# Kernel tuning notes

Measured on AMD Instinct MI355X. Metric: run time of the kernel, lower is better.

The kernel has to match this reference:

```python
import jax, jax.numpy as jnp
import numpy as np

V, D, B, L = 100000, 64, 4096, 200

def setup_inputs() -> dict:
    key = jax.random.key(0)
    ks = jax.random.split(key, 10)
    s = 0.05  # keep activations in a sane range for sigmoid
    return {
        "item_ids": jax.random.randint(ks[0], (B,), 0, V),
        "history": jax.random.randint(ks[1], (B, L), 0, V),
        "hist_len": jax.random.randint(ks[2], (B,), 1, L + 1),
        "emb_table": jax.random.normal(ks[3], (V, D), jnp.float32) * s,
        "aW1": jax.random.normal(ks[4], (3 * D, D), jnp.float32) * s,
        "ab1": jnp.zeros((D,), jnp.float32),
        "aW2": jax.random.normal(ks[5], (D, 1), jnp.float32) * s,
        "ab2": jnp.zeros((1,), jnp.float32),
        "fW1": jax.random.normal(ks[6], (3 * D, 128), jnp.float32) * s,
        "fb1": jnp.zeros((128,), jnp.float32),
        "fW2": jax.random.normal(ks[7], (128, 64), jnp.float32) * s,
        "fb2": jnp.zeros((64,), jnp.float32),
        "fW3": jax.random.normal(ks[8], (64, 1), jnp.float32) * s,
        "fb3": jnp.zeros((1,), jnp.float32),
    }

def reference(item_ids, history, hist_len, emb_table, aW1, ab1, aW2, ab2,
              fW1, fb1, fW2, fb2, fW3, fb3):
    target = emb_table[item_ids]                      # [B, D]
    hist = emb_table[history]                         # [B, L, D]
    # original pads short histories with zero rows -> zero the padded tail
    mask = (jnp.arange(hist.shape[1])[None, :] < hist_len[:, None]).astype(hist.dtype)
    hist = hist * mask[..., None]
    tgt = jnp.broadcast_to(target[:, None, :], hist.shape)     # [B, L, D]
    # attention_fc takes 3*D features: (hist, target, hist*target)
    feat = jnp.concatenate([hist, tgt, hist * tgt], axis=-1)   # [B, L, 3D]
    h = jax.nn.relu(feat @ aW1 + ab1)                 # [B, L, D]
    scores = (h @ aW2 + ab2)[..., 0]                  # [B, L]
    # faithful to original: softmax over full padded length (no length mask)
    w = jax.nn.softmax(scores, axis=1)
    pooled = jnp.einsum('bl,bld->bd', w, hist)        # [B, D]
    comb = jnp.concatenate([target, pooled, pooled - target], axis=-1)  # [B, 3D]
    z = jax.nn.relu(comb @ fW1 + fb1)
    z = jax.nn.relu(z @ fW2 + fb2)
    return jax.nn.sigmoid(z @ fW3 + fb3)              # [B, 1]
```

## Files before the change

### kernel.cpp

```cpp
#include <hip/hip_runtime.h>
#include <hip/hip_bf16.h>

#define NV 100000
#define ND 64
#define NB 4096
#define NL 200
#define HST 72

typedef __bf16 bf16_t;
typedef __bf16 bf16x8 __attribute__((ext_vector_type(8)));
typedef float  f32x4  __attribute__((ext_vector_type(4)));

__global__ __launch_bounds__(256, 5)
void din_kernel1(const int* __restrict__ item_ids,
                 const int* __restrict__ history,
                 const int* __restrict__ hist_len,
                 const float* __restrict__ emb,
                 const float* __restrict__ aW1,
                 const float* __restrict__ ab1,
                 const float* __restrict__ aW2,
                 float* __restrict__ comb_ws)
{
    __shared__ __align__(16) bf16_t histA[208 * HST];
    __shared__ __align__(16) float sc_w[208];
    __shared__ float pp[256];
    __shared__ float tgt[64];
    __shared__ float cb[64];
    __shared__ float pooled[64];
    __shared__ float red[8];

    const int b    = blockIdx.x;
    const int tid  = threadIdx.x;
    const int item = item_ids[b];
    const int len  = hist_len[b];
    const int wave = tid >> 6, lane = tid & 63;
    const int col  = lane & 15, quad = lane >> 4;

    if (tid < 64) tgt[tid] = emb[(long)item * ND + tid];

    {
        const int p     = tid & 3;
        const int lbase = tid >> 2;
        int  idxs[4];
        bool vs[4];
        #pragma unroll
        for (int pass = 0; pass < 4; ++pass) {
            int l  = pass * 64 + lbase;
            int lc = l < NL ? l : NL - 1;
            idxs[pass] = history[b * NL + lc];
            vs[pass]   = l < len;
        }
        #pragma unroll
        for (int g = 0; g < 2; ++g) {
            f32x4 r[2][4];
            #pragma unroll
            for (int q = 0; q < 2; ++q) {
                int pass = g * 2 + q;
                int l = pass * 64 + lbase;
                if (l < 208 && vs[pass]) {
                    const float* src = emb + (long)idxs[pass] * ND + p * 16;
                    r[q][0] = *(const f32x4*)(src);
                    r[q][1] = *(const f32x4*)(src + 4);
                    r[q][2] = *(const f32x4*)(src + 8);
                    r[q][3] = *(const f32x4*)(src + 12);
                }
            }
            #pragma unroll
            for (int q = 0; q < 2; ++q) {
                int pass = g * 2 + q;
                int l = pass * 64 + lbase;
                if (l < 208) {
                    bf16x8 o0 = (bf16x8)(bf16_t)0.f, o1 = (bf16x8)(bf16_t)0.f;
                    if (vs[pass]) {
                        #pragma unroll
                        for (int i = 0; i < 4; ++i) {
                            o0[i]     = (bf16_t)r[q][0][i];
                            o0[i + 4] = (bf16_t)r[q][1][i];
                            o1[i]     = (bf16_t)r[q][2][i];
                            o1[i + 4] = (bf16_t)r[q][3][i];
                        }
                    }
                    bf16_t* dst = &histA[l * HST + p * 16];
                    *(bf16x8*)(dst)     = o0;
                    *(bf16x8*)(dst + 8) = o1;
                }
            }
        }
    }

    {
        const int n4 = (tid & 15) * 4;
        const int kp = tid >> 4;
        f32x4 t4  = *(const f32x4*)(emb + (long)item * ND + kp * 4);
        f32x4 wb0 = *(const f32x4*)(aW1 + (64 + kp * 4 + 0) * 64 + n4);
        f32x4 wb1 = *(const f32x4*)(aW1 + (64 + kp * 4 + 1) * 64 + n4);
        f32x4 wb2 = *(const f32x4*)(aW1 + (64 + kp * 4 + 2) * 64 + n4);
        f32x4 wb3 = *(const f32x4*)(aW1 + (64 + kp * 4 + 3) * 64 + n4);
        f32x4 c4;
        #pragma unroll
        for (int j = 0; j < 4; ++j)
            c4[j] = t4[0] * wb0[j] + t4[1] * wb1[j] + t4[2] * wb2[j] + t4[3] * wb3[j];
        #pragma unroll
        for (int j = 0; j < 4; ++j) {
            c4[j] += __shfl_xor(c4[j], 16, 64);
            c4[j] += __shfl_xor(c4[j], 32, 64);
        }
        if (lane < 16) *(f32x4*)&pp[wave * 64 + n4] = c4;
    }

    __syncthreads();

    if (tid < 64) cb[tid] = ab1[tid] + pp[tid] + pp[64 + tid] + pp[128 + tid] + pp[192 + tid];

    bf16x8 bfrag[4][2];
    #pragma unroll
    for (int kb = 0; kb < 2; ++kb) {
        f32x4 t0 = *(const f32x4*)&tgt[kb * 32 + quad * 8];
        f32x4 t1 = *(const f32x4*)&tgt[kb * 32 + quad * 8 + 4];
        #pragma unroll
        for (int nt = 0; nt < 4; ++nt) {
            const int n = nt * 16 + col;
            const float* pa = aW1 + (long)(kb * 32 + quad * 8) * 64 + n;
            const float* pc = pa + 128 * 64;
            float wa[8], wc[8];
            #pragma unroll
            for (int j = 0; j < 8; ++j) { wa[j] = pa[j * 64]; wc[j] = pc[j * 64]; }
            bf16x8 w;
            #pragma unroll
            for (int j = 0; j < 8; ++j) {
                float tk = (j < 4) ? t0[j] : t1[j - 4];
                w[j] = (bf16_t)(wa[j] + tk * wc[j]);
            }
            bfrag[nt][kb] = w;
        }
    }
    float a2vals[4];
    #pragma unroll
    for (int nt = 0; nt < 4; ++nt) a2vals[nt] = aW2[nt * 16 + col];

    __syncthreads();
    float cvals[4];
    #pragma unroll
    for (int nt = 0; nt < 4; ++nt) cvals[nt] = cb[nt * 16 + col];

    for (int mt = wave; mt < 13; mt += 4) {
        const bf16_t* arow = &histA[(mt * 16 + col) * HST + quad * 8];
        bf16x8 af0 = *(const bf16x8*)(arow);
        bf16x8 af1 = *(const bf16x8*)(arow + 32);
        float sc[4] = {0.f, 0.f, 0.f, 0.f};
        #pragma unroll
        for (int nt = 0; nt < 4; ++nt) {
            f32x4 acc = {0.f, 0.f, 0.f, 0.f};
            acc = __builtin_amdgcn_mfma_f32_16x16x32_bf16(af0, bfrag[nt][0], acc, 0, 0, 0);
            acc = __builtin_amdgcn_mfma_f32_16x16x32_bf16(af1, bfrag[nt][1], acc, 0, 0, 0);
            #pragma unroll
            for (int i = 0; i < 4; ++i) {
                float h = acc[i] + cvals[nt];
                h = h > 0.f ? h : 0.f;
                sc[i] += h * a2vals[nt];
            }
        }
        #pragma unroll
        for (int off = 1; off < 16; off <<= 1)
            #pragma unroll
            for (int i = 0; i < 4; ++i) sc[i] += __shfl_xor(sc[i], off, 64);
        if (col == 0) {
            f32x4 outv = {sc[0], sc[1], sc[2], sc[3]};
            *(f32x4*)&sc_w[mt * 16 + quad * 4] = outv;
        }
    }
    __syncthreads();

    {
        float s = (tid < NL) ? sc_w[tid] : -1e30f;
        float m = s;
        #pragma unroll
        for (int off = 32; off > 0; off >>= 1) m = fmaxf(m, __shfl_xor(m, off, 64));
        if (lane == 0) red[wave] = m;
        __syncthreads();
        m = fmaxf(fmaxf(red[0], red[1]), fmaxf(red[2], red[3]));
        float e = (tid < NL) ? __expf(s - m) : 0.f;
        float ssum = e;
        #pragma unroll
        for (int off = 32; off > 0; off >>= 1) ssum += __shfl_xor(ssum, off, 64);
        if (lane == 0) red[4 + wave] = ssum;
        __syncthreads();
        float tot = red[4] + red[5] + red[6] + red[7];
        if (tid < NL) sc_w[tid] = e / tot;
    }
    __syncthreads();

    {
        float acc = 0.f;
        for (int l = wave; l < NL; l += 4)
            acc += sc_w[l] * (float)histA[l * HST + lane];
        pp[wave * 64 + lane] = acc;
    }
    __syncthreads();
    if (tid < 64) pooled[tid] = pp[tid] + pp[64 + tid] + pp[128 + tid] + pp[192 + tid];
    __syncthreads();

    if (tid < 192) {
        float v;
        if (tid < 64)       v = tgt[tid];
        else if (tid < 128) v = pooled[tid - 64];
        else                v = pooled[tid - 128] - tgt[tid - 128];
        comb_ws[(long)b * 192 + tid] = v;
    }
}

__global__ __launch_bounds__(256)
void din_kernel2(const float* __restrict__ comb,
                 const float* __restrict__ fW1, const float* __restrict__ fb1,
                 const float* __restrict__ fW2, const float* __restrict__ fb2,
                 const float* __restrict__ fW3, const float* __restrict__ fb3,
                 float* __restrict__ out)
{
    __shared__ float combs[4 * 192];
    __shared__ float z1s[4 * 128];
    const int tid = threadIdx.x;
    const int rb  = blockIdx.x * 4;

    for (int i = tid; i < 4 * 192; i += 256) combs[i] = comb[(long)rb * 192 + i];
    __syncthreads();

    {
        const int j  = tid & 127;
        const int r0 = (tid >> 7) * 2, r1 = r0 + 1;
        float a0 = fb1[j], a1 = a0;
        #pragma unroll 4
        for (int i = 0; i < 192; ++i) {
            float w = fW1[i * 128 + j];
            a0 += combs[r0 * 192 + i] * w;
            a1 += combs[r1 * 192 + i] * w;
        }
        z1s[r0 * 128 + j] = fmaxf(a0, 0.f);
        z1s[r1 * 128 + j] = fmaxf(a1, 0.f);
    }
    __syncthreads();

    {
        const int j2 = tid & 63;
        const int r2 = tid >> 6;
        float acc = fb2[j2];
        #pragma unroll 4
        for (int i = 0; i < 128; ++i)
            acc += z1s[r2 * 128 + i] * fW2[i * 64 + j2];
        float s = fmaxf(acc, 0.f) * fW3[j2];
        #pragma unroll
        for (int off = 1; off < 64; off <<= 1) s += __shfl_xor(s, off, 64);
        if (j2 == 0) out[rb + r2] = 1.f / (1.f + __expf(-(s + fb3[0])));
    }
}

extern "C" void kernel_launch(void* const* d_in, const int* in_sizes, int n_in,
                              void* d_out, int out_size, void* d_ws, size_t ws_size,
                              hipStream_t stream) {
    const int*   item_ids = (const int*)d_in[0];
    const int*   history  = (const int*)d_in[1];
    const int*   hist_len = (const int*)d_in[2];
    const float* emb      = (const float*)d_in[3];
    const float* aW1      = (const float*)d_in[4];
    const float* ab1      = (const float*)d_in[5];
    const float* aW2      = (const float*)d_in[6];
    const float* fW1      = (const float*)d_in[8];
    const float* fb1      = (const float*)d_in[9];
    const float* fW2      = (const float*)d_in[10];
    const float* fb2      = (const float*)d_in[11];
    const float* fW3      = (const float*)d_in[12];
    const float* fb3      = (const float*)d_in[13];

    float* comb = (float*)d_ws;

    din_kernel1<<<NB, 256, 0, stream>>>(item_ids, history, hist_len, emb,
                                        aW1, ab1, aW2, comb);
    din_kernel2<<<NB / 4, 256, 0, stream>>>(comb, fW1, fb1, fW2, fb2, fW3, fb3,
                                            (float*)d_out);
}
```

Measured before the change: 166.2 us.

## Pre-convert embedding table to bf16 and gather half-width rows

Adds a pre-pass kernel that converts the whole fp32 embedding table into a bf16 copy in workspace on every call. The attention kernel then gathers history rows from that copy, halving the bytes moved per gathered row and dropping the in-kernel conversion. The price is a full read of the table plus a half-size write each call, and an extra kernel launch. The old fp32 gather path is kept as a fallback when the workspace is too small.

Result: slower. 169.6 us (+2.0%).

```diff
diff --git a/kernel.cpp b/kernel.cpp
--- a/kernel.cpp
+++ b/kernel.cpp
@@ -11,11 +11,25 @@
 typedef __bf16 bf16x8 __attribute__((ext_vector_type(8)));
 typedef float  f32x4  __attribute__((ext_vector_type(4)));
 
+__global__ __launch_bounds__(256)
+void din_cvt(const float* __restrict__ emb, bf16_t* __restrict__ embh)
+{
+    const long base = ((long)blockIdx.x * 256 + threadIdx.x) * 8;
+    f32x4 a0 = *(const f32x4*)(emb + base);
+    f32x4 a1 = *(const f32x4*)(emb + base + 4);
+    bf16x8 o;
+    #pragma unroll
+    for (int i = 0; i < 4; ++i) { o[i] = (bf16_t)a0[i]; o[i + 4] = (bf16_t)a1[i]; }
+    *(bf16x8*)(embh + base) = o;
+}
+
+template <bool BT>
 __global__ __launch_bounds__(256, 5)
 void din_kernel1(const int* __restrict__ item_ids,
                  const int* __restrict__ history,
                  const int* __restrict__ hist_len,
                  const float* __restrict__ emb,
+                 const bf16_t* __restrict__ embh,
                  const float* __restrict__ aW1,
                  const float* __restrict__ ab1,
                  const float* __restrict__ aW2,
@@ -38,16 +52,41 @@
 
     if (tid < 64) tgt[tid] = emb[(long)item * ND + tid];
 
-    {
+    if constexpr (BT) {
+        const int p  = tid & 1;
+        const int lb = tid >> 1;
+        const int l1 = 128 + lb;
+        const int i0 = history[b * NL + (lb < NL ? lb : NL - 1)];
+        const int i1 = history[b * NL + (l1 < NL ? l1 : NL - 1)];
+        const bool v0 = lb < len, v1 = l1 < len;
+        const bf16x8 z = (bf16x8)(bf16_t)0.f;
+        bf16x8 r0[4] = {z, z, z, z}, r1[4] = {z, z, z, z};
+        if (v0) {
+            const bf16_t* s = embh + (long)i0 * ND + p * 32;
+            #pragma unroll
+            for (int j = 0; j < 4; ++j) r0[j] = *(const bf16x8*)(s + j * 8);
+        }
+        if (v1) {
+            const bf16_t* s = embh + (long)i1 * ND + p * 32;
+            #pragma unroll
+            for (int j = 0; j < 4; ++j) r1[j] = *(const bf16x8*)(s + j * 8);
+        }
+        bf16_t* d0 = &histA[lb * HST + p * 32];
+        #pragma unroll
+        for (int j = 0; j < 4; ++j) *(bf16x8*)(d0 + j * 8) = r0[j];
+        if (l1 < 208) {
+            bf16_t* d1 = &histA[l1 * HST + p * 32];
+            #pragma unroll
+            for (int j = 0; j < 4; ++j) *(bf16x8*)(d1 + j * 8) = r1[j];
+        }
+    } else {
         const int p     = tid & 3;
         const int lbase = tid >> 2;
-        int  idxs[4];
-        bool vs[4];
+        int  idxs[4]; bool vs[4];
         #pragma unroll
         for (int pass = 0; pass < 4; ++pass) {
             int l  = pass * 64 + lbase;
-            int lc = l < NL ? l : NL - 1;
-            idxs[pass] = history[b * NL + lc];
+            idxs[pass] = history[b * NL + (l < NL ? l : NL - 1)];
             vs[pass]   = l < len;
         }
         #pragma unroll
@@ -55,33 +94,27 @@
             f32x4 r[2][4];
             #pragma unroll
             for (int q = 0; q < 2; ++q) {
-                int pass = g * 2 + q;
-                int l = pass * 64 + lbase;
+                int pass = g * 2 + q, l = pass * 64 + lbase;
                 if (l < 208 && vs[pass]) {
                     const float* src = emb + (long)idxs[pass] * ND + p * 16;
-                    r[q][0] = *(const f32x4*)(src);
-                    r[q][1] = *(const f32x4*)(src + 4);
-                    r[q][2] = *(const f32x4*)(src + 8);
-                    r[q][3] = *(const f32x4*)(src + 12);
+                    #pragma unroll
+                    for (int j = 0; j < 4; ++j) r[q][j] = *(const f32x4*)(src + j * 4);
                 }
             }
             #pragma unroll
             for (int q = 0; q < 2; ++q) {
-                int pass = g * 2 + q;
-                int l = pass * 64 + lbase;
+                int pass = g * 2 + q, l = pass * 64 + lbase;
                 if (l < 208) {
                     bf16x8 o0 = (bf16x8)(bf16_t)0.f, o1 = (bf16x8)(bf16_t)0.f;
                     if (vs[pass]) {
                         #pragma unroll
                         for (int i = 0; i < 4; ++i) {
-                            o0[i]     = (bf16_t)r[q][0][i];
-                            o0[i + 4] = (bf16_t)r[q][1][i];
-                            o1[i]     = (bf16_t)r[q][2][i];
-                            o1[i + 4] = (bf16_t)r[q][3][i];
+                            o0[i] = (bf16_t)r[q][0][i]; o0[i + 4] = (bf16_t)r[q][1][i];
+                            o1[i] = (bf16_t)r[q][2][i]; o1[i + 4] = (bf16_t)r[q][3][i];
                         }
                     }
                     bf16_t* dst = &histA[l * HST + p * 16];
-                    *(bf16x8*)(dst)     = o0;
+                    *(bf16x8*)(dst) = o0;
                     *(bf16x8*)(dst + 8) = o1;
                 }
             }
@@ -270,10 +303,23 @@
     const float* fW3      = (const float*)d_in[12];
     const float* fb3      = (const float*)d_in[13];
 
-    float* comb = (float*)d_ws;
-
-    din_kernel1<<<NB, 256, 0, stream>>>(item_ids, history, hist_len, emb,
-                                        aW1, ab1, aW2, comb);
-    din_kernel2<<<NB / 4, 256, 0, stream>>>(comb, fW1, fb1, fW2, fb2, fW3, fb3,
-                                            (float*)d_out);
+    const size_t embh_bytes = (size_t)NV * ND * sizeof(bf16_t);
+    const size_t comb_bytes = (size_t)NB * 192 * sizeof(float);
+    const bool   use_bt     = ws_size >= embh_bytes + comb_bytes;
+
+    if (use_bt) {
+        bf16_t* embh = (bf16_t*)d_ws;
+        float*  comb = (float*)((char*)d_ws + embh_bytes);
+        din_cvt<<<(NV * ND) / (256 * 8), 256, 0, stream>>>(emb, embh);
+        din_kernel1<true><<<NB, 256, 0, stream>>>(item_ids, history, hist_len, emb,
+                                                  embh, aW1, ab1, aW2, comb);
+        din_kernel2<<<NB / 4, 256, 0, stream>>>(comb, fW1, fb1, fW2, fb2, fW3, fb3,
+                                                (float*)d_out);
+    } else {
+        float* comb = (float*)d_ws;
+        din_kernel1<false><<<NB, 256, 0, stream>>>(item_ids, history, hist_len, emb,
+                                                   (const bf16_t*)nullptr, aW1, ab1, aW2, comb);
+        din_kernel2<<<NB / 4, 256, 0, stream>>>(comb, fW1, fb1, fW2, fb2, fW3, fb3,
+                                                (float*)d_out);
+    }
 }
```
